# Performance work log

Hardware: AMD Instinct MI355X
Metric: run time of the kernel (lower is better)

## Reference

```python
import jax, jax.numpy as jnp
import numpy as np

N_HEADS = 16
NEG_INF = jnp.float32(-1e9)


def split_heads(x, h):
    # (b, t, h*d) -> (b*h, t, d)
    b, t, e = x.shape
    return x.reshape(b, t, h, e // h).transpose(0, 2, 1, 3).reshape(b * h, t, e // h)


def setup_inputs() -> dict:
    key = jax.random.key(0)
    ks = jax.random.split(key, 8)
    B, T, E = 1, 2048, 1024
    QK, V, NB, ML = 1024, 1024, 10, 2048
    g = lambda k, shp, sc: jax.random.normal(k, shp, jnp.float32) * sc
    return {
        "X_bte": g(ks[0], (B, T, E), 1.0),
        "W_q": g(ks[1], (E, QK), 0.02),
        "b_q": jnp.zeros((QK,), jnp.float32),
        "W_k": g(ks[2], (E, QK), 0.02),
        "W_v": g(ks[3], (E, V), 0.02),
        "W_proj": g(ks[4], (V, E), 0.02),
        "b_proj": jnp.zeros((E,), jnp.float32),
        "W_r": g(ks[5], (E, NB * N_HEADS), 0.02),
        "b_r": jnp.zeros((NB * N_HEADS,), jnp.float32),
        "b_nd": g(ks[6], (NB, ML), 0.2),  # B_SCALE = 0.2
    }


def relattn_logits(X_bte, W_r, b_r, b_nd):
    # R_btn: per-head mixing coefficients over the n_basis banded bias rows
    R_btn = split_heads(X_bte @ W_r + b_r, N_HEADS)      # (B*h, t, n_basis)
    t = R_btn.shape[1]
    T = t  # self-attention, no cache
    max_len = b_nd.shape[1]
    # Fused form of einsum('btn,ntT->btT', R, bandify(b_nd,t,T)):
    # first contract bases, then gather the Toeplitz diagonal d = i - j.
    P_btd = jnp.einsum('btn,nd->btd', R_btn, b_nd)       # (B*h, t, max_len)
    i = jnp.arange(t)[:, None]
    j = jnp.arange(T)[None, :]
    rel = i - j                                          # time difference
    valid = (rel >= 0) & (rel < max_len)
    idx = jnp.clip(rel, 0, max_len - 1)
    extra_btT = jnp.where(valid, P_btd[:, i, idx], jnp.float32(0.0))
    return extra_btT                                     # (B*h, t, T)


def reference(X_bte, W_q, b_q, W_k, W_v, W_proj, b_proj, W_r, b_r, b_nd):
    B, t, _ = X_bte.shape
    Q = split_heads(X_bte @ W_q + b_q, N_HEADS)          # (B*h, t, dqk)
    K = split_heads(X_bte @ W_k, N_HEADS)                # k_layer has no bias
    Vh = split_heads(X_bte @ W_v, N_HEADS)               # v_layer has no bias
    d = Q.shape[-1]

    extra_btT = relattn_logits(X_bte, W_r, b_r, b_nd)
    logits = jnp.einsum('bqd,bkd->bqk', Q, K) / jnp.sqrt(jnp.float32(d)) + extra_btT
    causal = jnp.tril(jnp.ones((t, t), bool))
    logits = jnp.where(causal, logits, NEG_INF)
    A = jax.nn.softmax(logits, axis=-1)                  # (B*h, t, t)
    out = jnp.einsum('bqk,bkd->bqd', A, Vh)              # (B*h, t, dv)
    out = out.reshape(B, N_HEADS, t, -1).transpose(0, 2, 1, 3).reshape(B, t, -1)
    return out @ W_proj + b_proj                          # (B, t, x_size)
```

## Files before the change

kernel.cpp:

```cpp
#include <hip/hip_runtime.h>
#include <hip/hip_bf16.h>
#include <math.h>


typedef __attribute__((ext_vector_type(8))) short bf16x8;
typedef __attribute__((ext_vector_type(4))) float f32x4;
typedef unsigned long long __attribute__((may_alias)) u64a;

#define MFMA16(a,b,c) __builtin_amdgcn_mfma_f32_16x16x32_bf16((a),(b),(c),0,0,0)
#define GLB(p)  ((const __attribute__((address_space(1))) void*)(p))
#define LDSP(p) ((__attribute__((address_space(3))) void*)(p))
#define LDY2 3328
#define LOG2E 1.44269504088896f

__device__ __forceinline__ unsigned short f2bf(float x){
  unsigned u = __float_as_uint(x);
  u = (u + 0x7FFFu + ((u >> 16) & 1u)) >> 16;
  return (unsigned short)u;
}
__device__ __forceinline__ unsigned short f2bf_rn(float x){
  __hip_bfloat16 b = __float2bfloat16(x);
  return *reinterpret_cast<unsigned short*>(&b);
}
__device__ __forceinline__ float bf2f(unsigned short b){
  return __uint_as_float(((unsigned)b) << 16);
}


__global__ __launch_bounds__(256) void prep_mega(
    const float* __restrict__ X,
    const float* __restrict__ Wq, const float* __restrict__ Wk,
    const float* __restrict__ Wv, const float* __restrict__ Wr,
    const float* __restrict__ Wp,
    const float* __restrict__ bq, const float* __restrict__ br,
    unsigned short* __restrict__ Xb, unsigned short* __restrict__ WbT,
    unsigned short* __restrict__ WpT, float* __restrict__ bias)
{
  __shared__ float tile[64][65];
  const int b = blockIdx.x;
  const int tid = threadIdx.x;

  if (b < 1024){
    const int i = (b * 256 + tid) * 8;
    f32x4 a = *(const f32x4*)(X + i);
    f32x4 v2 = *(const f32x4*)(X + i + 4);
    bf16x8 v;
    v[0]=(short)f2bf(a.x); v[1]=(short)f2bf(a.y); v[2]=(short)f2bf(a.z); v[3]=(short)f2bf(a.w);
    v[4]=(short)f2bf(v2.x); v[5]=(short)f2bf(v2.y); v[6]=(short)f2bf(v2.z); v[7]=(short)f2bf(v2.w);
    *(bf16x8*)(Xb + i) = v;
    return;
  }
  if (b < 1024 + 832){
    const int idx = b - 1024;
    const int k0 = (idx & 15) * 64, c0 = (idx >> 4) * 64;
    {
      const int r = tid >> 2, cs = (tid & 3) << 4;
      #pragma unroll
      for (int q = 0; q < 4; ++q){
        const int c = c0 + cs + q * 4;
        f32x4 v;
        if (c < 1024){
          v = *(const f32x4*)(Wq + (size_t)(k0+r)*1024 + c);
          const float s = 0.125f * LOG2E;
          v.x *= s; v.y *= s; v.z *= s; v.w *= s;
        }
        else if (c < 2048) v = *(const f32x4*)(Wk + (size_t)(k0+r)*1024 + (c-1024));
        else if (c < 3072) v = *(const f32x4*)(Wv + (size_t)(k0+r)*1024 + (c-2048));
        else if (c < 3232) v = *(const f32x4*)(Wr + (size_t)(k0+r)*160  + (c-3072));
        else               v = (f32x4){0.f,0.f,0.f,0.f};
        tile[r][cs+q*4+0]=v.x; tile[r][cs+q*4+1]=v.y; tile[r][cs+q*4+2]=v.z; tile[r][cs+q*4+3]=v.w;
      }
    }
    __syncthreads();
    const int c = tid >> 2, ks = (tid & 3) << 4;
    bf16x8 o0, o1;
    #pragma unroll
    for (int x = 0; x < 8; ++x) o0[x] = (short)f2bf(tile[ks + x][c]);
    #pragma unroll
    for (int x = 0; x < 8; ++x) o1[x] = (short)f2bf(tile[ks + 8 + x][c]);
    *(bf16x8*)(WbT + (size_t)(c0 + c) * 1024 + k0 + ks)     = o0;
    *(bf16x8*)(WbT + (size_t)(c0 + c) * 1024 + k0 + ks + 8) = o1;
    return;
  }
  if (b < 1024 + 832 + 256){
    const int idx = b - 1856;
    const int k0 = (idx & 15) * 64, c0 = (idx >> 4) * 64;
    {
      const int r = tid >> 2, cs = (tid & 3) << 4;
      #pragma unroll
      for (int q = 0; q < 4; ++q){
        f32x4 v = *(const f32x4*)(Wp + (size_t)(k0+r)*1024 + c0 + cs + q*4);
        tile[r][cs+q*4+0]=v.x; tile[r][cs+q*4+1]=v.y; tile[r][cs+q*4+2]=v.z; tile[r][cs+q*4+3]=v.w;
      }
    }
    __syncthreads();
    const int c = tid >> 2, ks = (tid & 3) << 4;
    bf16x8 o0, o1;
    #pragma unroll
    for (int x = 0; x < 8; ++x) o0[x] = (short)f2bf(tile[ks + x][c]);
    #pragma unroll
    for (int x = 0; x < 8; ++x) o1[x] = (short)f2bf(tile[ks + 8 + x][c]);
    *(bf16x8*)(WpT + (size_t)(c0 + c) * 1024 + k0 + ks)     = o0;
    *(bf16x8*)(WpT + (size_t)(c0 + c) * 1024 + k0 + ks + 8) = o1;
    return;
  }
  const int c = (b - 2112) * 256 + tid;
  if (c < 3328){
    float v = 0.f;
    if (c < 1024) v = bq[c] * 0.125f * LOG2E;
    else if (c >= 3072 && c < 3232) v = br[c - 3072];
    bias[c] = v;
  }
}


__global__ __launch_bounds__(256) void post_mega(
    const unsigned short* __restrict__ Y, const float* __restrict__ bnd,
    unsigned short* __restrict__ Vt, unsigned short* __restrict__ BndT)
{
  __shared__ unsigned short tile[64][72];
  const int b = blockIdx.x;
  const int tid = threadIdx.x;

  if (b < 512){
    const int h = b >> 5, t0 = (b & 31) * 64;
    {
      const int r = tid >> 2, cs = (tid & 3) << 4;
      const unsigned short* src = Y + (size_t)(t0 + r) * LDY2 + 2048 + h * 64 + cs;
      *(bf16x8*)&tile[r][cs]     = *(const bf16x8*)src;
      *(bf16x8*)&tile[r][cs + 8] = *(const bf16x8*)(src + 8);
    }
    __syncthreads();
    const int d = tid >> 2, ts = (tid & 3) << 4;
    bf16x8 o0, o1;
    #pragma unroll
    for (int x = 0; x < 8; ++x) o0[x] = (short)tile[ts + x][d];
    #pragma unroll
    for (int x = 0; x < 8; ++x) o1[x] = (short)tile[ts + 8 + x][d];
    *(bf16x8*)(Vt + (size_t)(h*64 + d) * 2048 + t0 + ts)     = o0;
    *(bf16x8*)(Vt + (size_t)(h*64 + d) * 2048 + t0 + ts + 8) = o1;
    return;
  }
  const int t = (b - 512) * 256 + tid;
  if (t >= 2176) return;
  const int rel = t - 64;
  unsigned short* dst = BndT + (size_t)t * 32;
  bf16x8 v0 = {}, v1 = {}, z = {};
  if (rel >= 0 && rel < 2048){
    #pragma unroll
    for (int n = 0; n < 8; ++n) v0[n] = (short)f2bf(bnd[n * 2048 + rel] * LOG2E);
    v1[0] = (short)f2bf(bnd[8 * 2048 + rel] * LOG2E);
    v1[1] = (short)f2bf(bnd[9 * 2048 + rel] * LOG2E);
  }
  *(bf16x8*)dst        = v0;
  *(bf16x8*)(dst + 8)  = v1;
  *(bf16x8*)(dst + 16) = z;
  *(bf16x8*)(dst + 24) = z;
}


__global__ __launch_bounds__(256) void gemm64(
    const unsigned short* __restrict__ A,
    const unsigned short* __restrict__ BT,
    const float* __restrict__ bias,
    void* __restrict__ C, int ldc, int out_f32)
{
  __shared__ unsigned short As[64 * 64];
  __shared__ unsigned short Bs[128 * 64];
  const int tid = threadIdx.x;
  const int w = tid >> 6, lane = tid & 63;
  const int lid = lane & 15, lgrp = lane >> 4;
  const int wm = w >> 1, wn = w & 1;
  const int row0 = blockIdx.y << 6, col0 = blockIdx.x << 7;
  const int sr = lane >> 3;
  const int sc = (lane & 7) ^ sr;

  f32x4 acc[2][4] = {};

  for (int k0 = 0; k0 < 1024; k0 += 64){
    #pragma unroll
    for (int it = 0; it < 2; ++it){
      const int r0w = (w << 4) + (it << 3);
      const int r = r0w + sr;
      __builtin_amdgcn_global_load_lds(GLB(A + (size_t)(row0 + r) * 1024 + k0 + (sc << 3)),
                                       LDSP(&As[r0w << 6]), 16, 0, 0);
    }
    #pragma unroll
    for (int it = 0; it < 4; ++it){
      const int r0w = (w << 5) + (it << 3);
      const int r = r0w + sr;
      __builtin_amdgcn_global_load_lds(GLB(BT + (size_t)(col0 + r) * 1024 + k0 + (sc << 3)),
                                       LDSP(&Bs[r0w << 6]), 16, 0, 0);
    }
    __syncthreads();

    bf16x8 af[2][2], bfr[4][2];
    #pragma unroll
    for (int m = 0; m < 2; ++m){
      const int ra = wm * 32 + m * 16 + lid;
      #pragma unroll
      for (int kk = 0; kk < 2; ++kk){
        const int kc = kk * 4 + lgrp;
        af[m][kk] = *(const bf16x8*)&As[(ra << 6) + ((kc ^ (lid & 7)) << 3)];
      }
    }
    #pragma unroll
    for (int n = 0; n < 4; ++n){
      const int rb = wn * 64 + n * 16 + lid;
      #pragma unroll
      for (int kk = 0; kk < 2; ++kk){
        const int kc = kk * 4 + lgrp;
        bfr[n][kk] = *(const bf16x8*)&Bs[(rb << 6) + ((kc ^ (lid & 7)) << 3)];
      }
    }
    #pragma unroll
    for (int m = 0; m < 2; ++m)
      #pragma unroll
      for (int n = 0; n < 4; ++n){
        acc[m][n] = MFMA16(af[m][0], bfr[n][0], acc[m][n]);
        acc[m][n] = MFMA16(af[m][1], bfr[n][1], acc[m][n]);
      }
    __syncthreads();
  }

  #pragma unroll
  for (int m = 0; m < 2; ++m){
    #pragma unroll
    for (int n = 0; n < 4; ++n){
      const int col = col0 + wn * 64 + n * 16 + lid;
      const float bv = bias[col];
      #pragma unroll
      for (int i = 0; i < 4; ++i){
        const int row = row0 + wm * 32 + m * 16 + lgrp * 4 + i;
        const float v = acc[m][n][i] + bv;
        if (out_f32) ((float*)C)[(size_t)row * ldc + col] = v;
        else ((unsigned short*)C)[(size_t)row * ldc + col] = f2bf(v);
      }
    }
  }
}


__device__ __forceinline__ void stage_tile(
    const unsigned short* __restrict__ Y,
    const unsigned short* __restrict__ Vt,
    unsigned short* __restrict__ Ksb,
    unsigned short* __restrict__ Vsb,
    int j0, int h, int sr, int scc)
{
  #pragma unroll
  for (int st = 0; st < 8; ++st){
    const int r0w = st * 8;
    const int r = r0w + sr;
    __builtin_amdgcn_global_load_lds(
        GLB(Y + (size_t)(j0 + r) * LDY2 + 1024 + h*64 + (scc << 3)),
        LDSP(&Ksb[r0w << 6]), 16, 0, 0);
    __builtin_amdgcn_global_load_lds(
        GLB(Vt + (size_t)(h*64 + r) * 2048 + j0 + (scc << 3)),
        LDSP(&Vsb[r0w << 6]), 16, 0, 0);
  }
}

__device__ __forceinline__ void attn_tile_body(
    const unsigned short* __restrict__ Ksb,
    const unsigned short* __restrict__ Vsb,
    unsigned short* __restrict__ un,
    const bf16x8 (&bw)[5],
    const bf16x8 (&qf)[2], const bf16x8& rf,
    int lid, int lgrp,
    bool diag, int ql,
    float& m_i, float& l_i, f32x4 (&o)[4])
{
  f32x4 s[4] = {};
  __builtin_amdgcn_s_setprio(1);
  #pragma unroll
  for (int kk = 0; kk < 2; ++kk){
    const int kc = kk * 4 + lgrp;
    #pragma unroll
    for (int n4 = 0; n4 < 4; ++n4){
      const bf16x8 kf = *(const bf16x8*)&Ksb[((n4*16 + lid) << 6) + ((kc ^ (lid & 7)) << 3)];
      s[n4] = MFMA16(kf, qf[kk], s[n4]);
    }
  }
  __builtin_amdgcn_s_setprio(0);

  #pragma unroll
  for (int f = 0; f < 5; ++f){
    f32x4 ef = {};
    ef = MFMA16(rf, bw[f], ef);
    const unsigned lo = ((unsigned)f2bf_rn(ef[0])) | (((unsigned)f2bf_rn(ef[1])) << 16);
    const unsigned hi = ((unsigned)f2bf_rn(ef[2])) | (((unsigned)f2bf_rn(ef[3])) << 16);
    const unsigned long long pk = ((unsigned long long)hi << 32) | lo;
    *(u64a*)&un[(f*16 + lid) * 20 + lgrp*4] = pk;
  }

  #pragma unroll
  for (int n4 = 0; n4 < 4; ++n4){
    #pragma unroll
    for (int i = 0; i < 4; ++i){
      const int jl = n4*16 + lgrp*4 + i;
      float v = s[n4][i] + bf2f(un[(lid - jl + 63) * 20 + lid]);
      if (diag && jl > ql) v = -1e9f;
      s[n4][i] = v;
    }
  }

  float rm = s[0][0];
  #pragma unroll
  for (int n4 = 0; n4 < 4; ++n4)
    #pragma unroll
    for (int i = 0; i < 4; ++i) rm = fmaxf(rm, s[n4][i]);
  rm = fmaxf(rm, __shfl_xor(rm, 16));
  rm = fmaxf(rm, __shfl_xor(rm, 32));

  if (__all(rm - m_i <= 11.54f)){
    float rs = 0.f;
    #pragma unroll
    for (int n4 = 0; n4 < 4; ++n4)
      #pragma unroll
      for (int i = 0; i < 4; ++i){
        const float pv = __builtin_amdgcn_exp2f(s[n4][i] - m_i);
        s[n4][i] = pv;
        rs += pv;
      }
    rs += __shfl_xor(rs, 16);
    rs += __shfl_xor(rs, 32);
    l_i += rs;
  } else {
    const float mn = fmaxf(m_i, rm);
    const float sc_ = __builtin_amdgcn_exp2f(m_i - mn);
    m_i = mn;
    float rs = 0.f;
    #pragma unroll
    for (int n4 = 0; n4 < 4; ++n4)
      #pragma unroll
      for (int i = 0; i < 4; ++i){
        const float pv = __builtin_amdgcn_exp2f(s[n4][i] - mn);
        s[n4][i] = pv;
        rs += pv;
      }
    rs += __shfl_xor(rs, 16);
    rs += __shfl_xor(rs, 32);
    l_i = l_i * sc_ + rs;
    #pragma unroll
    for (int n4 = 0; n4 < 4; ++n4)
      #pragma unroll
      for (int i = 0; i < 4; ++i) o[n4][i] *= sc_;
  }

  #pragma unroll
  for (int n4 = 0; n4 < 4; ++n4){
    const unsigned a = ((unsigned)f2bf_rn(s[n4][0])) | (((unsigned)f2bf_rn(s[n4][1])) << 16);
    const unsigned b = ((unsigned)f2bf_rn(s[n4][2])) | (((unsigned)f2bf_rn(s[n4][3])) << 16);
    const int chunk = (n4*2 + (lgrp >> 1)) ^ (lid & 7);
    const int base = (lid << 6) + (chunk << 3) + ((lgrp & 1) << 2);
    *(unsigned*)&un[base]     = a;
    *(unsigned*)&un[base + 2] = b;
  }

  __builtin_amdgcn_s_setprio(1);
  #pragma unroll
  for (int kk = 0; kk < 2; ++kk){
    const int kc = kk * 4 + lgrp;
    const bf16x8 pb = *(const bf16x8*)&un[(lid << 6) + ((kc ^ (lid & 7)) << 3)];
    #pragma unroll
    for (int n4 = 0; n4 < 4; ++n4){
      const bf16x8 vf = *(const bf16x8*)&Vsb[((n4*16 + lid) << 6) + ((kc ^ (lid & 7)) << 3)];
      o[n4] = MFMA16(vf, pb, o[n4]);
    }
  }
  __builtin_amdgcn_s_setprio(0);
}

__global__ __launch_bounds__(128) void attn_mfma(
    const unsigned short* __restrict__ Y,
    const unsigned short* __restrict__ Vt,
    const unsigned short* __restrict__ BndT,
    unsigned short* __restrict__ AO)
{
  __shared__ unsigned short KV[4][4096];
  __shared__ unsigned short UN[2][1600];

  const int id = blockIdx.x;
  const int h = id & 15;
  const int u = (id >> 4) & 3;
  const int tid = threadIdx.x;
  const int grp = tid >> 6;
  const int lane = tid & 63;
  const int lid = lane & 15, lgrp = lane >> 4;
  const int sr = lane >> 3;
  const int scc = (lane & 7) ^ sr;

  unsigned short* Ksg = &KV[grp][0];
  unsigned short* Vsg = &KV[2 + grp][0];
  unsigned short* un  = &UN[grp][0];

  const int ql = u * 16 + lid;

  #pragma unroll
  for (int seg = 0; seg < 2; ++seg){
    const int qb = seg ? (id >> 6) : (31 - (id >> 6));
    const int q0w = qb * 64 + u * 16;
    const int qrow = q0w + lid;
    const int nt = qb + 1;
    const int L = (nt + 1) >> 1;

    bf16x8 qf[2];
    #pragma unroll
    for (int kk = 0; kk < 2; ++kk)
      qf[kk] = *(const bf16x8*)(Y + (size_t)qrow * LDY2 + h*64 + ((kk*4 + lgrp) << 3));
    bf16x8 rf = {};
    {
      const unsigned* rp = (const unsigned*)(Y + (size_t)qrow * LDY2 + 3072 + h*10);
      if (lgrp == 0){
        #pragma unroll
        for (int x = 0; x < 4; ++x) ((unsigned*)&rf)[x] = rp[x];
      } else if (lgrp == 1){
        ((unsigned*)&rf)[0] = rp[4];
      }
    }

    float m_i = -INFINITY, l_i = 0.f;
    f32x4 o[4] = {};

    for (int it = 0; it < L; ++it){
      const int kb = 2 * it + grp;
      if (kb < nt){
        const int j0 = kb << 6;
        const int d0 = q0w - j0;

        stage_tile(Y, Vt, Ksg, Vsg, j0, h, sr, scc);

        bf16x8 bw[5];
        #pragma unroll
        for (int f = 0; f < 5; ++f){
          const int rowt = d0 + 1 + f * 16 + lid;
          bw[f] = *(const bf16x8*)(BndT + ((size_t)rowt << 5) + (lgrp << 3));
        }

        asm volatile("s_waitcnt vmcnt(0)" ::: "memory");
        __builtin_amdgcn_sched_barrier(0);

        attn_tile_body(Ksg, Vsg, un, bw, qf, rf, lid, lgrp,
                       kb == qb, ql, m_i, l_i, o);
      }
    }

    float* oScr  = (float*)&KV[1][0];
    float* mlScr = (float*)&KV[3][0];
    if (grp == 1){
      #pragma unroll
      for (int n4 = 0; n4 < 4; ++n4)
        *(f32x4*)&oScr[lid * 64 + n4*16 + lgrp*4] = o[n4];
      if (lgrp == 0){
        mlScr[lid * 2 + 0] = m_i;
        mlScr[lid * 2 + 1] = l_i;
      }
    }
    __syncthreads();
    if (grp == 0){
      const float m1 = mlScr[lid * 2 + 0];
      const float l1 = mlScr[lid * 2 + 1];
      const float M  = fmaxf(m_i, m1);
      const float a  = __builtin_amdgcn_exp2f(m_i - M);
      const float b  = __builtin_amdgcn_exp2f(m1 - M);
      const float inv = 1.f / (l_i * a + l1 * b);
      unsigned short* dst = AO + (size_t)qrow * 1024 + h * 64;
      #pragma unroll
      for (int n4 = 0; n4 < 4; ++n4){
        const f32x4 o1 = *(const f32x4*)&oScr[lid * 64 + n4*16 + lgrp*4];
        const float v0 = (o[n4][0]*a + o1[0]*b) * inv;
        const float v1 = (o[n4][1]*a + o1[1]*b) * inv;
        const float v2 = (o[n4][2]*a + o1[2]*b) * inv;
        const float v3 = (o[n4][3]*a + o1[3]*b) * inv;
        unsigned r0 = ((unsigned)f2bf_rn(v0)) | (((unsigned)f2bf_rn(v1)) << 16);
        unsigned r1 = ((unsigned)f2bf_rn(v2)) | (((unsigned)f2bf_rn(v3)) << 16);
        unsigned long long pk = ((unsigned long long)r1 << 32) | r0;
        *(u64a*)(dst + n4*16 + lgrp*4) = pk;
      }
    }
    __syncthreads();
  }
}


extern "C" void kernel_launch(void* const* d_in, const int* in_sizes, int n_in,
                              void* d_out, int out_size, void* d_ws, size_t ws_size,
                              hipStream_t stream) {
  const float* X   = (const float*)d_in[0];
  const float* Wq  = (const float*)d_in[1];
  const float* bq  = (const float*)d_in[2];
  const float* Wk  = (const float*)d_in[3];
  const float* Wv  = (const float*)d_in[4];
  const float* Wp  = (const float*)d_in[5];
  const float* bp  = (const float*)d_in[6];
  const float* Wr  = (const float*)d_in[7];
  const float* br  = (const float*)d_in[8];
  const float* bnd = (const float*)d_in[9];
  float* out = (float*)d_out;

  unsigned short* Xb  = (unsigned short*)d_ws;
  unsigned short* WbT = Xb  + (size_t)2048 * 1024;
  unsigned short* Yb  = WbT + (size_t)3328 * 1024;
  unsigned short* Vt  = Yb  + (size_t)2048 * 3328;
  unsigned short* WpT = Vt  + (size_t)1024 * 2048;
  float* bias = (float*)(WpT + (size_t)1024 * 1024);
  unsigned short* AO   = Xb;
  unsigned short* BndT = WbT + (size_t)3232 * 1024;

  prep_mega <<<2125,         256, 0, stream>>>(X, Wq, Wk, Wv, Wr, Wp, bq, br,
                                               Xb, WbT, WpT, bias);
  gemm64    <<<dim3(26, 32), 256, 0, stream>>>(Xb, WbT, bias, Yb, 3328, 0);
  post_mega <<<521,          256, 0, stream>>>(Yb, bnd, Vt, BndT);
  attn_mfma <<<1024,         128, 0, stream>>>(Yb, Vt, BndT, AO);
  gemm64    <<<dim3(8, 32),  256, 0, stream>>>(AO, WpT, bp, out, 1024, 1);
}
```

Before: 100.2 us.

## Fuse V transpose into QKV GEMM epilogue and fold band prep into prep kernel

The post_mega kernel is removed. The V-transpose is now written directly from the QKV GEMM epilogue as packed 4-element stores into Vt, and the BndT preparation moves into prep_mega as extra blocks. WbT writes are guarded so the padded rows past 3232, where BndT now lives, are not overwritten. The attention tile body is templated on the diagonal flag so off-diagonal tiles skip the mask check. This saves one kernel launch and the re-read of V from Y, at the cost of scattered 8-byte transposed stores in the GEMM epilogue.

After: 98.02 us, median of 2. 2.2% less time.

```diff
diff --git a/kernel.cpp b/kernel.cpp
--- a/kernel.cpp
+++ b/kernel.cpp
@@ -33,8 +33,10 @@
     const float* __restrict__ Wv, const float* __restrict__ Wr,
     const float* __restrict__ Wp,
     const float* __restrict__ bq, const float* __restrict__ br,
+    const float* __restrict__ bnd,
     unsigned short* __restrict__ Xb, unsigned short* __restrict__ WbT,
-    unsigned short* __restrict__ WpT, float* __restrict__ bias)
+    unsigned short* __restrict__ WpT, float* __restrict__ bias,
+    unsigned short* __restrict__ BndT)
 {
   __shared__ float tile[64][65];
   const int b = blockIdx.x;
@@ -73,13 +75,15 @@
     }
     __syncthreads();
     const int c = tid >> 2, ks = (tid & 3) << 4;
-    bf16x8 o0, o1;
-    #pragma unroll
-    for (int x = 0; x < 8; ++x) o0[x] = (short)f2bf(tile[ks + x][c]);
-    #pragma unroll
-    for (int x = 0; x < 8; ++x) o1[x] = (short)f2bf(tile[ks + 8 + x][c]);
-    *(bf16x8*)(WbT + (size_t)(c0 + c) * 1024 + k0 + ks)     = o0;
-    *(bf16x8*)(WbT + (size_t)(c0 + c) * 1024 + k0 + ks + 8) = o1;
+    if (c0 + c < 3232){
+      bf16x8 o0, o1;
+      #pragma unroll
+      for (int x = 0; x < 8; ++x) o0[x] = (short)f2bf(tile[ks + x][c]);
+      #pragma unroll
+      for (int x = 0; x < 8; ++x) o1[x] = (short)f2bf(tile[ks + 8 + x][c]);
+      *(bf16x8*)(WbT + (size_t)(c0 + c) * 1024 + k0 + ks)     = o0;
+      *(bf16x8*)(WbT + (size_t)(c0 + c) * 1024 + k0 + ks + 8) = o1;
+    }
     return;
   }
   if (b < 1024 + 832 + 256){
@@ -104,44 +108,17 @@
     *(bf16x8*)(WpT + (size_t)(c0 + c) * 1024 + k0 + ks + 8) = o1;
     return;
   }
-  const int c = (b - 2112) * 256 + tid;
-  if (c < 3328){
-    float v = 0.f;
-    if (c < 1024) v = bq[c] * 0.125f * LOG2E;
-    else if (c >= 3072 && c < 3232) v = br[c - 3072];
-    bias[c] = v;
-  }
-}
-
-
-__global__ __launch_bounds__(256) void post_mega(
-    const unsigned short* __restrict__ Y, const float* __restrict__ bnd,
-    unsigned short* __restrict__ Vt, unsigned short* __restrict__ BndT)
-{
-  __shared__ unsigned short tile[64][72];
-  const int b = blockIdx.x;
-  const int tid = threadIdx.x;
-
-  if (b < 512){
-    const int h = b >> 5, t0 = (b & 31) * 64;
-    {
-      const int r = tid >> 2, cs = (tid & 3) << 4;
-      const unsigned short* src = Y + (size_t)(t0 + r) * LDY2 + 2048 + h * 64 + cs;
-      *(bf16x8*)&tile[r][cs]     = *(const bf16x8*)src;
-      *(bf16x8*)&tile[r][cs + 8] = *(const bf16x8*)(src + 8);
-    }
-    __syncthreads();
-    const int d = tid >> 2, ts = (tid & 3) << 4;
-    bf16x8 o0, o1;
-    #pragma unroll
-    for (int x = 0; x < 8; ++x) o0[x] = (short)tile[ts + x][d];
-    #pragma unroll
-    for (int x = 0; x < 8; ++x) o1[x] = (short)tile[ts + 8 + x][d];
-    *(bf16x8*)(Vt + (size_t)(h*64 + d) * 2048 + t0 + ts)     = o0;
-    *(bf16x8*)(Vt + (size_t)(h*64 + d) * 2048 + t0 + ts + 8) = o1;
+  if (b < 2125){
+    const int c = (b - 2112) * 256 + tid;
+    if (c < 3328){
+      float v = 0.f;
+      if (c < 1024) v = bq[c] * 0.125f * LOG2E;
+      else if (c >= 3072 && c < 3232) v = br[c - 3072];
+      bias[c] = v;
+    }
     return;
   }
-  const int t = (b - 512) * 256 + tid;
+  const int t = (b - 2125) * 256 + tid;
   if (t >= 2176) return;
   const int rel = t - 64;
   unsigned short* dst = BndT + (size_t)t * 32;
@@ -163,7 +140,8 @@
     const unsigned short* __restrict__ A,
     const unsigned short* __restrict__ BT,
     const float* __restrict__ bias,
-    void* __restrict__ C, int ldc, int out_f32)
+    void* __restrict__ C, int ldc, int out_f32,
+    unsigned short* __restrict__ VtOut)
 {
   __shared__ unsigned short As[64 * 64];
   __shared__ unsigned short Bs[128 * 64];
@@ -174,6 +152,7 @@
   const int row0 = blockIdx.y << 6, col0 = blockIdx.x << 7;
   const int sr = lane >> 3;
   const int sc = (lane & 7) ^ sr;
+  const bool do_vt = (VtOut != nullptr) && (col0 >= 2048) && (col0 < 3072);
 
   f32x4 acc[2][4] = {};
 
@@ -229,12 +208,22 @@
     for (int n = 0; n < 4; ++n){
       const int col = col0 + wn * 64 + n * 16 + lid;
       const float bv = bias[col];
+      const int rowb = row0 + wm * 32 + m * 16 + lgrp * 4;
+      unsigned short bf[4];
       #pragma unroll
       for (int i = 0; i < 4; ++i){
-        const int row = row0 + wm * 32 + m * 16 + lgrp * 4 + i;
         const float v = acc[m][n][i] + bv;
-        if (out_f32) ((float*)C)[(size_t)row * ldc + col] = v;
-        else ((unsigned short*)C)[(size_t)row * ldc + col] = f2bf(v);
+        if (out_f32) ((float*)C)[(size_t)(rowb + i) * ldc + col] = v;
+        else {
+          bf[i] = f2bf(v);
+          ((unsigned short*)C)[(size_t)(rowb + i) * ldc + col] = bf[i];
+        }
+      }
+      if (do_vt){
+        const unsigned long long pk =
+            ((unsigned long long)bf[0])        | (((unsigned long long)bf[1]) << 16) |
+            (((unsigned long long)bf[2]) << 32) | (((unsigned long long)bf[3]) << 48);
+        *(u64a*)(VtOut + (size_t)(col - 2048) * 2048 + rowb) = pk;
       }
     }
   }
@@ -261,14 +250,14 @@
   }
 }
 
+template<bool DIAG>
 __device__ __forceinline__ void attn_tile_body(
     const unsigned short* __restrict__ Ksb,
     const unsigned short* __restrict__ Vsb,
     unsigned short* __restrict__ un,
     const bf16x8 (&bw)[5],
     const bf16x8 (&qf)[2], const bf16x8& rf,
-    int lid, int lgrp,
-    bool diag, int ql,
+    int lid, int lgrp, int ql,
     float& m_i, float& l_i, f32x4 (&o)[4])
 {
   f32x4 s[4] = {};
@@ -300,7 +289,7 @@
     for (int i = 0; i < 4; ++i){
       const int jl = n4*16 + lgrp*4 + i;
       float v = s[n4][i] + bf2f(un[(lid - jl + 63) * 20 + lid]);
-      if (diag && jl > ql) v = -1e9f;
+      if (DIAG && jl > ql) v = -1e9f;
       s[n4][i] = v;
     }
   }
@@ -441,8 +430,10 @@
         asm volatile("s_waitcnt vmcnt(0)" ::: "memory");
         __builtin_amdgcn_sched_barrier(0);
 
-        attn_tile_body(Ksg, Vsg, un, bw, qf, rf, lid, lgrp,
-                       kb == qb, ql, m_i, l_i, o);
+        if (kb == qb)
+          attn_tile_body<true >(Ksg, Vsg, un, bw, qf, rf, lid, lgrp, ql, m_i, l_i, o);
+        else
+          attn_tile_body<false>(Ksg, Vsg, un, bw, qf, rf, lid, lgrp, ql, m_i, l_i, o);
       }
     }
 
@@ -508,10 +499,9 @@
   unsigned short* AO   = Xb;
   unsigned short* BndT = WbT + (size_t)3232 * 1024;
 
-  prep_mega <<<2125,         256, 0, stream>>>(X, Wq, Wk, Wv, Wr, Wp, bq, br,
-                                               Xb, WbT, WpT, bias);
-  gemm64    <<<dim3(26, 32), 256, 0, stream>>>(Xb, WbT, bias, Yb, 3328, 0);
-  post_mega <<<521,          256, 0, stream>>>(Yb, bnd, Vt, BndT);
+  prep_mega <<<2134,         256, 0, stream>>>(X, Wq, Wk, Wv, Wr, Wp, bq, br, bnd,
+                                               Xb, WbT, WpT, bias, BndT);
+  gemm64    <<<dim3(26, 32), 256, 0, stream>>>(Xb, WbT, bias, Yb, 3328, 0, Vt);
   attn_mfma <<<1024,         128, 0, stream>>>(Yb, Vt, BndT, AO);
-  gemm64    <<<dim3(8, 32),  256, 0, stream>>>(AO, WpT, bp, out, 1024, 1);
-}
+  gemm64    <<<dim3(8, 32),  256, 0, stream>>>(AO, WpT, bp, out, 1024, 1, nullptr);
+}
```
